# Optimization experiments

Hardware: AMD Instinct MI355X
Metric: run time of the kernel (lower is better)

## Reference

```python
import jax, jax.numpy as jnp
import numpy as np

B, N, H, NH, P = 32, 400, 512, 8, 3
DK = H // NH
SCALE = DK ** -0.5
EPS = 1e-5


def _ln(x, g, b):
    m = jnp.mean(x, axis=-1, keepdims=True)
    v = jnp.mean((x - m) ** 2, axis=-1, keepdims=True)
    return (x - m) * jax.lax.rsqrt(v + EPS) * g + b


def _split(x):  # [B,N,H] -> [B,h,N,dk]
    return x.reshape(x.shape[0], x.shape[1], NH, DK).transpose(0, 2, 1, 3)


def _merge(x):  # [B,h,N,dk] -> [B,N,H]
    return x.transpose(0, 2, 1, 3).reshape(x.shape[0], x.shape[2], H)


def _attn(q, k, v, mask):
    s = jnp.einsum('bhid,bhjd->bhij', q, k) * SCALE
    s = s * (1.0 + mask[:, None])  # learned multiplicative prior mask
    p = jax.nn.softmax(s, axis=-1)
    return jnp.einsum('bhij,bhjd->bhid', p, v)


def _weight_gen(pri, z, C, wq, keys, wf, bf):
    # pooled token query attends over the num_priors prior matrices
    qv = jnp.mean(z @ wq, axis=1)  # [B,H]
    aw = jax.nn.softmax((qv @ keys.T) * (H ** -0.5), axis=-1)  # [B,P]
    w = jnp.einsum('bp,bpij->bij', aw, pri)  # [B,N,N] fused prior mask
    fused = jnp.einsum('bij,bjh->bih', C, z) @ wf + bf  # [B,N,H] neighborhood fusion
    return w, aw, fused


def _ffn(x, w1, b1, w2, b2):
    return jax.nn.gelu(x @ w1 + b1, approximate=False) @ w2 + b2


def _forward(x_FC, x_SC, pri_FC, pri_SC, FC, SC, dw,
             ln_attn_FC_g, ln_attn_FC_b, ln_attn_SC_g, ln_attn_SC_b,
             ln_ffn_FC_g, ln_ffn_FC_b, ln_ffn_SC_g, ln_ffn_SC_b,
             qkv_FC_w, qkv_SC_w,
             ffn_FC_w1, ffn_FC_b1, ffn_FC_w2, ffn_FC_b2,
             ffn_SC_w1, ffn_SC_b1, ffn_SC_w2, ffn_SC_b2,
             wg_q_w, wg_keys, wg_fuse_w, wg_fuse_b,
             dist_in_FC_w, dist_in_FC_b, dist_in_SC_w, dist_in_SC_b,
             dist_out_FC_w, dist_out_FC_b, dist_out_SC_w, dist_out_SC_b):
    z_FC = _ln(x_FC, ln_attn_FC_g, ln_attn_FC_b)
    z_SC = _ln(x_SC, ln_attn_SC_g, ln_attn_SC_b)
    q_FC, k_FC, v_FC = [_split(t) for t in jnp.split(z_FC @ qkv_FC_w, 3, axis=-1)]
    q_SC, k_SC, v_SC = [_split(t) for t in jnp.split(z_SC @ qkv_SC_w, 3, axis=-1)]
    w_FC, aw_FC, fused_FC = _weight_gen(pri_FC, z_FC, FC, wg_q_w, wg_keys, wg_fuse_w, wg_fuse_b)
    w_SC, aw_SC, fused_SC = _weight_gen(pri_SC, z_SC, SC, wg_q_w, wg_keys, wg_fuse_w, wg_fuse_b)
    ctx_FC = _merge(_attn(q_FC, k_FC, v_FC, w_FC))
    ctx_SC = _merge(_attn(q_SC, k_SC, v_SC, w_SC))
    attn_out_FC = x_FC + ctx_FC + fused_FC
    attn_out_SC = x_SC + ctx_SC + fused_SC
    x_FC_new = attn_out_FC + _ffn(_ln(attn_out_FC, ln_ffn_FC_g, ln_ffn_FC_b), ffn_FC_w1, ffn_FC_b1, ffn_FC_w2, ffn_FC_b2)
    x_SC_new = attn_out_SC + _ffn(_ln(attn_out_SC, ln_ffn_SC_g, ln_ffn_SC_b), ffn_SC_w1, ffn_SC_b1, ffn_SC_w2, ffn_SC_b2)
    wf, ws = dw[0], dw[1]
    proj_FC = x_FC_new @ dist_in_FC_w + dist_in_FC_b
    proj_SC = x_SC_new @ dist_in_SC_w + dist_in_SC_b
    l_FC = jax.nn.log_softmax(proj_FC.reshape(-1, H), axis=-1)
    l_SC = jax.nn.log_softmax(proj_SC.reshape(-1, H), axis=-1)
    p_FC = jnp.exp(l_FC)
    p_SC = jnp.exp(l_SC)
    rows = jnp.float32(l_FC.shape[0])
    kl_FC = jnp.sum(p_SC * (l_SC - l_FC)) / rows  # KLDiv(batchmean)(l_FC, p_SC)
    kl_SC = jnp.sum(p_FC * (l_FC - l_SC)) / rows
    x_FC_out = (1.0 - wf) * x_FC_new + wf * (proj_FC @ dist_out_FC_w + dist_out_FC_b)
    x_SC_out = (1.0 - ws) * x_SC_new + ws * (proj_SC @ dist_out_SC_w + dist_out_SC_b)
    distill_loss = 0.5 * (kl_FC * wf + kl_SC * ws)
    return (x_FC_out, x_SC_out, distill_loss, aw_FC, aw_SC)


def setup_inputs() -> dict:
    key = jax.random.key(0)
    ks = jax.random.split(key, 24)
    init = lambda k, shape: 0.02 * jax.random.normal(k, shape, jnp.float32)
    d = {}
    d['x_FC'] = jax.random.normal(ks[0], (B, N, H), jnp.float32)
    d['x_SC'] = jax.random.normal(ks[1], (B, N, H), jnp.float32)
    d['pri_FC'] = jax.random.uniform(ks[2], (B, P, N, N), jnp.float32)
    d['pri_SC'] = jax.random.uniform(ks[3], (B, P, N, N), jnp.float32)
    d['FC'] = jax.random.uniform(ks[4], (B, N, N), jnp.float32)
    d['SC'] = jax.random.uniform(ks[5], (B, N, N), jnp.float32)
    d['dw'] = jnp.array([0.5, 0.5], jnp.float32)
    for nm in ['ln_attn_FC', 'ln_attn_SC', 'ln_ffn_FC', 'ln_ffn_SC']:
        d[nm + '_g'] = jnp.ones((H,), jnp.float32)
        d[nm + '_b'] = jnp.zeros((H,), jnp.float32)
    d['qkv_FC_w'] = init(ks[6], (H, 3 * H))
    d['qkv_SC_w'] = init(ks[7], (H, 3 * H))
    d['ffn_FC_w1'] = init(ks[8], (H, 4 * H)); d['ffn_FC_b1'] = jnp.zeros((4 * H,), jnp.float32)
    d['ffn_FC_w2'] = init(ks[9], (4 * H, H)); d['ffn_FC_b2'] = jnp.zeros((H,), jnp.float32)
    d['ffn_SC_w1'] = init(ks[10], (H, 4 * H)); d['ffn_SC_b1'] = jnp.zeros((4 * H,), jnp.float32)
    d['ffn_SC_w2'] = init(ks[11], (4 * H, H)); d['ffn_SC_b2'] = jnp.zeros((H,), jnp.float32)
    d['wg_q_w'] = init(ks[12], (H, H))
    d['wg_keys'] = init(ks[13], (P, H))
    d['wg_fuse_w'] = init(ks[14], (H, H)); d['wg_fuse_b'] = jnp.zeros((H,), jnp.float32)
    d['dist_in_FC_w'] = init(ks[15], (H, H)); d['dist_in_FC_b'] = jnp.zeros((H,), jnp.float32)
    d['dist_in_SC_w'] = init(ks[16], (H, H)); d['dist_in_SC_b'] = jnp.zeros((H,), jnp.float32)
    d['dist_out_FC_w'] = init(ks[17], (H, H)); d['dist_out_FC_b'] = jnp.zeros((H,), jnp.float32)
    d['dist_out_SC_w'] = init(ks[18], (H, H)); d['dist_out_SC_b'] = jnp.zeros((H,), jnp.float32)
    return d


def reference(x_FC, x_SC, pri_FC, pri_SC, FC, SC, dw,
              ln_attn_FC_g, ln_attn_FC_b, ln_attn_SC_g, ln_attn_SC_b,
              ln_ffn_FC_g, ln_ffn_FC_b, ln_ffn_SC_g, ln_ffn_SC_b,
              qkv_FC_w, qkv_SC_w,
              ffn_FC_w1, ffn_FC_b1, ffn_FC_w2, ffn_FC_b2,
              ffn_SC_w1, ffn_SC_b1, ffn_SC_w2, ffn_SC_b2,
              wg_q_w, wg_keys, wg_fuse_w, wg_fuse_b,
              dist_in_FC_w, dist_in_FC_b, dist_in_SC_w, dist_in_SC_b,
              dist_out_FC_w, dist_out_FC_b, dist_out_SC_w, dist_out_SC_b):
    return _forward(x_FC, x_SC, pri_FC, pri_SC, FC, SC, dw,
                    ln_attn_FC_g, ln_attn_FC_b, ln_attn_SC_g, ln_attn_SC_b,
                    ln_ffn_FC_g, ln_ffn_FC_b, ln_ffn_SC_g, ln_ffn_SC_b,
                    qkv_FC_w, qkv_SC_w,
                    ffn_FC_w1, ffn_FC_b1, ffn_FC_w2, ffn_FC_b2,
                    ffn_SC_w1, ffn_SC_b1, ffn_SC_w2, ffn_SC_b2,
                    wg_q_w, wg_keys, wg_fuse_w, wg_fuse_b,
                    dist_in_FC_w, dist_in_FC_b, dist_in_SC_w, dist_in_SC_b,
                    dist_out_FC_w, dist_out_FC_b, dist_out_SC_w, dist_out_SC_b)
```

## Files before the change

### kernel.cpp

```cpp
#include <hip/hip_runtime.h>
#include <hip/hip_bf16.h>
#include <math.h>

typedef __hip_bfloat16 bf16;

#define B_  32
#define N_  400
#define H_  512
#define NH_ 8
#define DK_ 64
#define P_  3
#define BN_ (B_*N_)
#define H3_ 1536
#define H4_ 2048

#define GLD16(g, l) __builtin_amdgcn_global_load_lds( \
    (__attribute__((address_space(1))) void*)(g), \
    (__attribute__((address_space(3))) void*)(l), 16, 0, 0)

__device__ __forceinline__ float b2f(bf16 v){ return __bfloat162float(v); }
__device__ __forceinline__ bf16  f2b(float v){ return __float2bfloat16(v); }
__device__ __forceinline__ float bfu(unsigned short u){ return __uint_as_float(((unsigned int)u)<<16); }
__device__ __forceinline__ unsigned short f2bu(float v){
  union { bf16 b; unsigned short u; } cv; cv.b = __float2bfloat16(v); return cv.u;
}
__device__ __forceinline__ bool is_f32(const void* gref){
  return *(const unsigned int*)gref == 0x3F800000u;
}
__device__ __forceinline__ float ldRaw(const void* p, long i, bool f32){
  return f32 ? ((const float*)p)[i] : b2f(((const bf16*)p)[i]);
}
__device__ __forceinline__ void stRaw(void* p, long i, float v, bool f32){
  if (f32) ((float*)p)[i] = v; else ((bf16*)p)[i] = f2b(v);
}

__device__ __forceinline__ float waveSum(float v){
  #pragma unroll
  for (int o=32;o>0;o>>=1) v += __shfl_xor(v,o,64);
  return v;
}
__device__ __forceinline__ float waveMax(float v){
  #pragma unroll
  for (int o=32;o>0;o>>=1) v = fmaxf(v,__shfl_xor(v,o,64));
  return v;
}
__device__ __forceinline__ float blockSum(float v, float* wred){
  v = waveSum(v);
  int w = threadIdx.x>>6, l = threadIdx.x&63;
  if (l==0) wred[w]=v;
  __syncthreads();
  float r = wred[0]+wred[1]+wred[2]+wred[3];
  __syncthreads();
  return r;
}
__device__ __forceinline__ float blockMax(float v, float* wred){
  v = waveMax(v);
  int w = threadIdx.x>>6, l = threadIdx.x&63;
  if (l==0) wred[w]=v;
  __syncthreads();
  float r = fmaxf(fmaxf(wred[0],wred[1]),fmaxf(wred[2],wred[3]));
  __syncthreads();
  return r;
}

template<int XMODE>
__global__ __launch_bounds__(256)
void ln_kernel(const void* __restrict__ x, const void* __restrict__ g,
               const void* __restrict__ bb, bf16* __restrict__ out,
               const void* __restrict__ gref)
{
  __shared__ float wred[4];
  const bool F32 = is_f32(gref);
  long row = blockIdx.x;
  int t = threadIdx.x;
  long base = row*H_;
  float v0, v1;
  if (XMODE==0){ v0 = ldRaw(x, base+t, F32); v1 = ldRaw(x, base+t+256, F32); }
  else         { v0 = b2f(((const bf16*)x)[base+t]); v1 = b2f(((const bf16*)x)[base+t+256]); }
  float mean = blockSum(v0+v1, wred) * (1.f/512.f);
  float d0 = v0-mean, d1 = v1-mean;
  float var = blockSum(d0*d0+d1*d1, wred) * (1.f/512.f);
  float rs = rsqrtf(var + 1e-5f);
  bf16* orow = out + base;
  orow[t]     = f2b(d0*rs*ldRaw(g,t,F32)     + ldRaw(bb,t,F32));
  orow[t+256] = f2b(d1*rs*ldRaw(g,t+256,F32) + ldRaw(bb,t+256,F32));
}

struct TC6 {
  const float* W[6];
  bf16* WT[6];
  int K[6]; int N[6]; int base[6];
};
__global__ __launch_bounds__(256)
void tc6_kernel(TC6 p)
{
  __shared__ float tile[32][33];
  int gt = blockIdx.x;
  int seg = 0;
  #pragma unroll
  for (int i=1;i<6;++i) if (gt >= p.base[i]) seg = i;
  int lt = gt - p.base[seg];
  int K = p.K[seg], N = p.N[seg];
  int ntx = N >> 5;
  int n0 = (lt % ntx)*32, k0 = (lt / ntx)*32;
  const float* W = p.W[seg];
  bf16* WT = p.WT[seg];
  int t = threadIdx.x;
  int c = t & 31, r = t >> 5;
  #pragma unroll
  for (int q=0;q<4;++q){
    int k = r + q*8;
    tile[k][c] = W[(long)(k0+k)*N + n0 + c];
  }
  __syncthreads();
  #pragma unroll
  for (int q=0;q<4;++q){
    int nn = r + q*8;
    WT[(long)(n0+nn)*K + k0 + c] = f2b(tile[c][nn]);
  }
}

__global__ __launch_bounds__(256)
void ztrans_kernel(const bf16* __restrict__ ZB, bf16* __restrict__ ZBT)
{
  __shared__ unsigned short tile[32][33];
  int j0 = blockIdx.x*32, h0 = blockIdx.y*32, b = blockIdx.z;
  int t = threadIdx.x;
  int c = t & 31, r = t >> 5;
  const unsigned short* src = (const unsigned short*)(ZB + (long)b*N_*H_);
  #pragma unroll
  for (int p=0;p<4;++p){
    int j = j0 + r + p*8;
    unsigned short v = 0;
    if (j < 400) v = src[(long)j*H_ + h0 + c];
    tile[r+p*8][c] = v;
  }
  __syncthreads();
  unsigned short* dst = (unsigned short*)(ZBT + (long)b*512*416);
  #pragma unroll
  for (int p=0;p<4;++p){
    int hh = r + p*8;
    dst[(long)(h0+hh)*416 + j0 + c] = tile[c][hh];
  }
}

__global__ __launch_bounds__(256)
void cconv_kernel(const float* __restrict__ C, bf16* __restrict__ CB)
{
  long u = ((long)blockIdx.x*256 + threadIdx.x)*8;
  int b = (int)(u / (512*416));
  int rem = (int)(u - (long)b*(512*416));
  int r = rem / 416, c = rem % 416;
  ushort4 lo = {0,0,0,0}, hi = {0,0,0,0};
  if (r < 400 && c < 400){
    const float* p = C + (long)b*160000 + r*400 + c;
    float4 f0 = *(const float4*)p;
    float4 f1 = *(const float4*)(p+4);
    lo.x=f2bu(f0.x); lo.y=f2bu(f0.y); lo.z=f2bu(f0.z); lo.w=f2bu(f0.w);
    hi.x=f2bu(f1.x); hi.y=f2bu(f1.y); hi.z=f2bu(f1.z); hi.w=f2bu(f1.w);
  }
  *(ushort4*)((unsigned short*)CB + u)     = lo;
  *(ushort4*)((unsigned short*)CB + u + 4) = hi;
}

__global__ __launch_bounds__(256)
void vtrans_kernel(const bf16* __restrict__ qkv, bf16* __restrict__ vtg)
{
  __shared__ unsigned short tile[32][33];
  int j0 = blockIdx.x*32, d0 = blockIdx.y*32, bh = blockIdx.z;
  int b = bh >> 3, h = bh & 7;
  int t = threadIdx.x;
  int c = t & 31, r = t >> 5;
  const unsigned short* src = (const unsigned short*)(qkv + (long)b*N_*H3_ + 1024 + h*64 + d0);
  #pragma unroll
  for (int p=0;p<4;++p){
    int j = j0 + r + p*8;
    unsigned short v = 0;
    if (j < 400) v = src[(long)j*H3_ + c];
    tile[r+p*8][c] = v;
  }
  __syncthreads();
  unsigned short* dst = (unsigned short*)(vtg + (long)bh*64*416);
  #pragma unroll
  for (int p=0;p<4;++p){
    int dd = r + p*8;
    dst[(long)(d0+dd)*416 + j0 + c] = tile[c][dd];
  }
}

template<int MI,int ACT,int RES,int OMODE>
__global__ __launch_bounds__(256)
void mgemm_kernel(const bf16* __restrict__ A, const bf16* __restrict__ BT,
                  const float* __restrict__ bias, const bf16* __restrict__ res,
                  void* __restrict__ out, long oOff,
                  int M, int K, int Nn,
                  long sA, long sW, long sO,
                  const float* __restrict__ dwp, int dwidx)
{
  typedef __attribute__((ext_vector_type(8))) short bf16x8;
  typedef __attribute__((ext_vector_type(4))) float f32x4;
  constexpr int BM = MI*32;
  __shared__ unsigned short As[2][BM*32];
  __shared__ unsigned short Bs[2][128*32];
  int t = threadIdx.x;
  int w = t >> 6, l = t & 63;
  int wm = (w >> 1)*(MI*16), wn = (w & 1)*64;
  int m0 = blockIdx.y*BM, n0 = blockIdx.x*128;
  long zA = (long)blockIdx.z*sA;
  const bf16* Ab = A + zA;
  const bf16* Bb = BT + (long)blockIdx.z*sW;
  long zO = (long)blockIdx.z*sO;
  f32x4 acc[MI][4] = {};
  int lrow = l & 15, lkc = l >> 4;
  int srow = t >> 2, skc = t & 3;
  int sk = (skc ^ ((srow >> 1) & 3))*8;
  int ck = (lkc ^ ((lrow >> 1) & 3))*8;
  int nk = K >> 5;
  int buf = 0;

  #pragma unroll
  for (int half=0; half<MI/2; ++half){
    const unsigned short* gA = (const unsigned short*)Ab + (long)(m0+srow+half*64)*K + sk;
    GLD16(gA, &As[0][w*512 + half*2048]);
  }
  #pragma unroll
  for (int half=0; half<2; ++half){
    const unsigned short* gB = (const unsigned short*)Bb + (long)(n0+srow+half*64)*K + sk;
    GLD16(gB, &Bs[0][w*512 + half*2048]);
  }
  __syncthreads();
  for (int kt=0; kt<nk; ++kt){
    if (kt+1 < nk){
      int k1 = (kt+1) << 5;
      #pragma unroll
      for (int half=0; half<MI/2; ++half){
        const unsigned short* gA = (const unsigned short*)Ab + (long)(m0+srow+half*64)*K + k1 + sk;
        GLD16(gA, &As[buf^1][w*512 + half*2048]);
      }
      #pragma unroll
      for (int half=0; half<2; ++half){
        const unsigned short* gB = (const unsigned short*)Bb + (long)(n0+srow+half*64)*K + k1 + sk;
        GLD16(gB, &Bs[buf^1][w*512 + half*2048]);
      }
    }
    bf16x8 af[MI], bf_[4];
    #pragma unroll
    for (int i=0;i<MI;++i) af[i]  = *(const bf16x8*)&As[buf][(wm + i*16 + lrow)*32 + ck];
    #pragma unroll
    for (int i=0;i<4;++i)  bf_[i] = *(const bf16x8*)&Bs[buf][(wn + i*16 + lrow)*32 + ck];
    #pragma unroll
    for (int mi=0;mi<MI;++mi)
      #pragma unroll
      for (int ni=0;ni<4;++ni)
        acc[mi][ni] = __builtin_amdgcn_mfma_f32_16x16x32_bf16(bf_[ni], af[mi], acc[mi][ni], 0, 0, 0);
    __syncthreads();
    buf ^= 1;
  }
  float wbl = (RES==2) ? dwp[dwidx] : 0.f;
  #pragma unroll
  for (int mi=0;mi<MI;++mi){
    int gm = m0 + wm + mi*16 + lrow;
    if (gm >= M) continue;
    #pragma unroll
    for (int ni=0;ni<4;++ni){
      int gnb = n0 + wn + ni*16 + lkc*4;
      long o = zO + (long)gm*Nn + gnb;
      float v0 = acc[mi][ni][0], v1 = acc[mi][ni][1], v2 = acc[mi][ni][2], v3 = acc[mi][ni][3];
      if (bias){
        float4 bv = *(const float4*)&bias[gnb];
        v0 += bv.x; v1 += bv.y; v2 += bv.z; v3 += bv.w;
      }
      if (ACT==1){
        v0 = 0.5f*v0*(1.f + erff(v0*0.70710678118654752f));
        v1 = 0.5f*v1*(1.f + erff(v1*0.70710678118654752f));
        v2 = 0.5f*v2*(1.f + erff(v2*0.70710678118654752f));
        v3 = 0.5f*v3*(1.f + erff(v3*0.70710678118654752f));
      }
      if (RES==1){
        ushort4 r4 = *(const ushort4*)((const unsigned short*)res + o);
        v0 += bfu(r4.x); v1 += bfu(r4.y); v2 += bfu(r4.z); v3 += bfu(r4.w);
      }
      if (RES==2){
        ushort4 r4 = *(const ushort4*)((const unsigned short*)res + o);
        v0 = (1.f-wbl)*bfu(r4.x) + wbl*v0;
        v1 = (1.f-wbl)*bfu(r4.y) + wbl*v1;
        v2 = (1.f-wbl)*bfu(r4.z) + wbl*v2;
        v3 = (1.f-wbl)*bfu(r4.w) + wbl*v3;
      }
      if (OMODE==0){
        ushort4 o4;
        o4.x = f2bu(v0); o4.y = f2bu(v1); o4.z = f2bu(v2); o4.w = f2bu(v3);
        *(ushort4*)((unsigned short*)out + o) = o4;
      } else {
        *(float4*)((float*)out + oOff + o) = make_float4(v0,v1,v2,v3);
      }
    }
  }
}

__global__ __launch_bounds__(256)
void zbar_kernel(const bf16* __restrict__ Z, float* __restrict__ zbar)
{
  __shared__ float red[256];
  int hc = blockIdx.x, b = blockIdx.y;
  int t = threadIdx.x;
  int col = hc*64 + (t & 63), ns = t >> 6;
  const bf16* p = Z + (long)b*N_*H_ + (long)ns*100*H_ + col;
  float s = 0.f;
  for (int n=0;n<100;++n) s += b2f(p[(long)n*H_]);
  red[t] = s;
  __syncthreads();
  if (t < 64){
    float tot = red[t]+red[t+64]+red[t+128]+red[t+192];
    zbar[b*512 + hc*64 + t] = tot * (1.f/400.f);
  }
}

__global__ __launch_bounds__(256)
void qv_kernel(const float* __restrict__ zbar, const void* __restrict__ wq,
               float* __restrict__ qv, const void* __restrict__ gref)
{
  __shared__ float red[256];
  const bool F32 = is_f32(gref);
  int ch = blockIdx.x, b = blockIdx.y;
  int t = threadIdx.x;
  int col = ch*32 + (t & 31), ks = t >> 5;
  const float* zb = zbar + b*512;
  float s = 0.f;
  int k0 = ks*64;
  for (int k=0;k<64;++k)
    s = fmaf(zb[k0+k], ldRaw(wq, (long)(k0+k)*512 + col, F32), s);
  red[t] = s;
  __syncthreads();
  if (t < 32){
    float q = 0.f;
    #pragma unroll
    for (int i=0;i<8;++i) q += red[t + i*32];
    qv[b*512 + ch*32 + t] = q;
  }
}

__global__ __launch_bounds__(256)
void aw_kernel(const float* __restrict__ qv, const void* __restrict__ keys,
               float* __restrict__ awf, void* __restrict__ outbase, long offAw,
               const void* __restrict__ gref)
{
  __shared__ float wred[4];
  const bool F32 = is_f32(gref);
  int b = blockIdx.x, t = threadIdx.x;
  const float* q = qv + b*512;
  float lg[3];
  #pragma unroll
  for (int p=0;p<3;++p){
    float part = q[t]*ldRaw(keys, p*512+t, F32) + q[t+256]*ldRaw(keys, p*512+t+256, F32);
    lg[p] = blockSum(part, wred) * 0.04419417382415922f;
  }
  float m = fmaxf(lg[0], fmaxf(lg[1], lg[2]));
  float e0 = expf(lg[0]-m), e1 = expf(lg[1]-m), e2 = expf(lg[2]-m);
  float inv = 1.f/(e0+e1+e2);
  if (t<3){
    float a = (t==0?e0:(t==1?e1:e2))*inv;
    awf[b*3+t] = a;
    stRaw(outbase, offAw + b*3 + t, a, F32);
  }
}

__global__ __launch_bounds__(256)
void wcomb_kernel(const void* __restrict__ pri, const float* __restrict__ awf,
                  bf16* __restrict__ WM, const void* __restrict__ gref)
{
  const bool F32 = is_f32(gref);
  long u = (long)blockIdx.x*256 + threadIdx.x;
  long e0 = u*4;
  int b = (int)(e0 / 160000);
  long r = e0 - (long)b*160000;
  float a0 = awf[b*3+0], a1 = awf[b*3+1], a2 = awf[b*3+2];
  float o0,o1,o2,o3;
  if (F32){
    const float* p0 = (const float*)pri + (long)b*3*160000 + r;
    float4 a = *(const float4*)(p0);
    float4 c = *(const float4*)(p0 + 160000);
    float4 d = *(const float4*)(p0 + 320000);
    o0 = a0*a.x + a1*c.x + a2*d.x;
    o1 = a0*a.y + a1*c.y + a2*d.y;
    o2 = a0*a.z + a1*c.z + a2*d.z;
    o3 = a0*a.w + a1*c.w + a2*d.w;
  } else {
    const bf16* p0 = (const bf16*)pri + (long)b*3*160000 + r;
    ushort4 a = *(const ushort4*)(p0);
    ushort4 c = *(const ushort4*)(p0 + 160000);
    ushort4 d = *(const ushort4*)(p0 + 320000);
    o0 = a0*bfu(a.x) + a1*bfu(c.x) + a2*bfu(d.x);
    o1 = a0*bfu(a.y) + a1*bfu(c.y) + a2*bfu(d.y);
    o2 = a0*bfu(a.z) + a1*bfu(c.z) + a2*bfu(d.z);
    o3 = a0*bfu(a.w) + a1*bfu(c.w) + a2*bfu(d.w);
  }
  ushort4 o;
  o.x = f2bu(o0); o.y = f2bu(o1); o.z = f2bu(o2); o.w = f2bu(o3);
  *(ushort4*)(WM + e0) = o;
}

__global__ __launch_bounds__(128)
void attn_kernel(const bf16* __restrict__ qkv, const bf16* __restrict__ wm,
                 const bf16* __restrict__ vtg, const void* __restrict__ x,
                 const bf16* __restrict__ fused, bf16* __restrict__ aout,
                 const void* __restrict__ gref)
{
  typedef __attribute__((ext_vector_type(8))) short bf16x8;
  typedef __attribute__((ext_vector_type(4))) float f32x4;
  __shared__ unsigned short Pbuf[2][2][16*40];
  const bool F32 = is_f32(gref);
  int t = threadIdx.x, wv = t >> 6, l = t & 63;
  int h = blockIdx.x, b = blockIdx.y;
  int qt = blockIdx.z*2 + wv;
  if (qt >= 25) return;
  int lr = l & 15, lg = l >> 4;
  int i0 = qt*16;
  const bf16* qb = qkv + (long)b*N_*H3_ + h*64;
  const bf16* kb = qb + 512;
  const bf16* wrow = wm + (long)b*N_*N_;
  const bf16* vt = vtg + (long)(b*NH_ + h)*64*416;
  bf16x8 qf0 = *(const bf16x8*)(qb + (long)(i0+lr)*H3_ + lg*8);
  bf16x8 qf1 = *(const bf16x8*)(qb + (long)(i0+lr)*H3_ + 32 + lg*8);
  float rm = -1e30f, rl = 0.f;
  f32x4 o[4] = {};
  #pragma unroll
  for (int w=0; w<13; ++w){
    int t0 = 2*w, t1 = 2*w+1;
    f32x4 s0, s1;
    {
      bf16x8 kf0 = *(const bf16x8*)(kb + (long)(t0*16+lr)*H3_ + lg*8);
      bf16x8 kf1 = *(const bf16x8*)(kb + (long)(t0*16+lr)*H3_ + 32 + lg*8);
      f32x4 st = {0.f,0.f,0.f,0.f};
      st = __builtin_amdgcn_mfma_f32_16x16x32_bf16(kf0, qf0, st, 0,0,0);
      st = __builtin_amdgcn_mfma_f32_16x16x32_bf16(kf1, qf1, st, 0,0,0);
      uint2 w4 = *(const uint2*)(wrow + (long)(i0+lr)*400 + t0*16 + lg*4);
      s0[0] = st[0]*0.125f*(1.f + bfu((unsigned short)(w4.x & 0xffffu)));
      s0[1] = st[1]*0.125f*(1.f + bfu((unsigned short)(w4.x >> 16)));
      s0[2] = st[2]*0.125f*(1.f + bfu((unsigned short)(w4.y & 0xffffu)));
      s0[3] = st[3]*0.125f*(1.f + bfu((unsigned short)(w4.y >> 16)));
    }
    if (t1 < 25){
      bf16x8 kf0 = *(const bf16x8*)(kb + (long)(t1*16+lr)*H3_ + lg*8);
      bf16x8 kf1 = *(const bf16x8*)(kb + (long)(t1*16+lr)*H3_ + 32 + lg*8);
      f32x4 st = {0.f,0.f,0.f,0.f};
      st = __builtin_amdgcn_mfma_f32_16x16x32_bf16(kf0, qf0, st, 0,0,0);
      st = __builtin_amdgcn_mfma_f32_16x16x32_bf16(kf1, qf1, st, 0,0,0);
      uint2 w4 = *(const uint2*)(wrow + (long)(i0+lr)*400 + t1*16 + lg*4);
      s1[0] = st[0]*0.125f*(1.f + bfu((unsigned short)(w4.x & 0xffffu)));
      s1[1] = st[1]*0.125f*(1.f + bfu((unsigned short)(w4.x >> 16)));
      s1[2] = st[2]*0.125f*(1.f + bfu((unsigned short)(w4.y & 0xffffu)));
      s1[3] = st[3]*0.125f*(1.f + bfu((unsigned short)(w4.y >> 16)));
    } else {
      s1[0]=s1[1]=s1[2]=s1[3] = -1e30f;
    }
    float tm = fmaxf(fmaxf(fmaxf(s0[0],s0[1]), fmaxf(s0[2],s0[3])),
                     fmaxf(fmaxf(s1[0],s1[1]), fmaxf(s1[2],s1[3])));
    tm = fmaxf(tm, __shfl_xor(tm, 16));
    tm = fmaxf(tm, __shfl_xor(tm, 32));
    float mn = fmaxf(rm, tm);
    float sc = __expf(rm - mn);
    unsigned pk0x, pk0y, pk1x = 0u, pk1y = 0u;
    float ls = 0.f;
    {
      unsigned u0 = f2bu(__expf(s0[0]-mn)), u1 = f2bu(__expf(s0[1]-mn));
      unsigned u2 = f2bu(__expf(s0[2]-mn)), u3 = f2bu(__expf(s0[3]-mn));
      pk0x = u0 | (u1<<16); pk0y = u2 | (u3<<16);
      ls += __uint_as_float(u0<<16) + __uint_as_float(u1<<16)
          + __uint_as_float(u2<<16) + __uint_as_float(u3<<16);
    }
    if (t1 < 25){
      unsigned u0 = f2bu(__expf(s1[0]-mn)), u1 = f2bu(__expf(s1[1]-mn));
      unsigned u2 = f2bu(__expf(s1[2]-mn)), u3 = f2bu(__expf(s1[3]-mn));
      pk1x = u0 | (u1<<16); pk1y = u2 | (u3<<16);
      ls += __uint_as_float(u0<<16) + __uint_as_float(u1<<16)
          + __uint_as_float(u2<<16) + __uint_as_float(u3<<16);
    }
    ls += __shfl_xor(ls, 16);
    ls += __shfl_xor(ls, 32);
    rl = rl*sc + ls;
    rm = mn;
    unsigned short* pb = Pbuf[wv][w & 1];
    *(uint2*)&pb[lr*40 + lg*4]      = make_uint2(pk0x, pk0y);
    *(uint2*)&pb[lr*40 + 16 + lg*4] = make_uint2(pk1x, pk1y);
    bf16x8 pa = *(const bf16x8*)&pb[lr*40 + lg*8];
    float sq0 = __shfl(sc, lg*4 + 0);
    float sq1 = __shfl(sc, lg*4 + 1);
    float sq2 = __shfl(sc, lg*4 + 2);
    float sq3 = __shfl(sc, lg*4 + 3);
    #pragma unroll
    for (int dt=0; dt<4; ++dt){
      o[dt][0] *= sq0; o[dt][1] *= sq1; o[dt][2] *= sq2; o[dt][3] *= sq3;
      bf16x8 vf = *(const bf16x8*)(vt + (long)(dt*16+lr)*416 + w*32 + lg*8);
      o[dt] = __builtin_amdgcn_mfma_f32_16x16x32_bf16(pa, vf, o[dt], 0,0,0);
    }
  }
  float invl = 1.f/rl;
  #pragma unroll
  for (int q=0;q<4;++q){
    float iv = __shfl(invl, lg*4 + q);
    long gi = (long)(b*N_ + i0 + lg*4 + q);
    #pragma unroll
    for (int dt=0;dt<4;++dt){
      long oi = gi*H_ + h*64 + dt*16 + lr;
      float xv = F32 ? ((const float*)x)[oi] : b2f(((const bf16*)x)[oi]);
      float fv = b2f(fused[oi]);
      aout[oi] = f2b(o[dt][q]*iv + xv + fv);
    }
  }
}

__global__ __launch_bounds__(256)
void kl_rows_kernel(const bf16* __restrict__ pF, const bf16* __restrict__ pS,
                    float2* __restrict__ rowpart)
{
  __shared__ float wred[4];
  long row = blockIdx.x;
  int t = threadIdx.x;
  const bf16* fr = pF + row*512;
  const bf16* sr = pS + row*512;
  float f0 = b2f(fr[t]), f1 = b2f(fr[t+256]), s0 = b2f(sr[t]), s1 = b2f(sr[t+256]);
  float mF = blockMax(fmaxf(f0,f1), wred);
  float mS = blockMax(fmaxf(s0,s1), wred);
  float sumF = blockSum(__expf(f0-mF)+__expf(f1-mF), wred);
  float sumS = blockSum(__expf(s0-mS)+__expf(s1-mS), wred);
  float lseF = mF + __logf(sumF), lseS = mS + __logf(sumS);
  float lF0 = f0-lseF, lF1 = f1-lseF, lS0 = s0-lseS, lS1 = s1-lseS;
  float pS0 = __expf(lS0), pS1 = __expf(lS1), pF0 = __expf(lF0), pF1 = __expf(lF1);
  float a  = pS0*(lS0-lF0) + pS1*(lS1-lF1);
  float bb = pF0*(lF0-lS0) + pF1*(lF1-lS1);
  a  = blockSum(a,  wred);
  bb = blockSum(bb, wred);
  if (t==0) rowpart[row] = make_float2(a, bb);
}

__global__ __launch_bounds__(256)
void kl_final_kernel(const float2* __restrict__ rowpart, const void* __restrict__ dw,
                     void* __restrict__ outbase, long offLoss,
                     const void* __restrict__ gref)
{
  __shared__ float wred[4];
  const bool F32 = is_f32(gref);
  int t = threadIdx.x;
  float sa=0.f, sb=0.f;
  for (int i=t;i<BN_;i+=256){ float2 v = rowpart[i]; sa+=v.x; sb+=v.y; }
  sa = blockSum(sa, wred);
  sb = blockSum(sb, wred);
  if (t==0){
    float wf = ldRaw(dw,0,F32), ws = ldRaw(dw,1,F32);
    float loss = 0.5f*((sa/12800.f)*wf + (sb/12800.f)*ws);
    stRaw(outbase, offLoss, loss, F32);
  }
}

#define OFF_ZB    0L
#define OFF_QKV   13107200L
#define OFF_FUSED 52428800L
#define OFF_WM    65536000L
#define OFF_CZ    75776000L
#define OFF_PROJ0 88883200L
#define OFF_PROJ1 101990400L
#define OFF_QKVT  115097600L
#define OFF_W1T   116670464L
#define OFF_W2T   118767616L
#define OFF_FUT   120864768L
#define OFF_DIT   121389056L
#define OFF_DOT   121913344L
#define OFF_ZBT   122437632L
#define OFF_ZBAR  136069120L
#define OFF_AWF   136134656L
#define OFF_ROWP  136135680L
#define OFF_VTG   136238080L
#define OFF_QV    149869568L

extern "C" void kernel_launch(void* const* d_in, const int* in_sizes, int n_in,
                              void* d_out, int out_size, void* d_ws, size_t ws_size,
                              hipStream_t stream)
{
  (void)in_sizes; (void)n_in; (void)out_size; (void)ws_size;
  const void* x[2]    = {d_in[0],  d_in[1]};
  const void* pri[2]  = {d_in[2],  d_in[3]};
  const float* Cm[2]  = {(const float*)d_in[4], (const float*)d_in[5]};
  const float* dwf    =  (const float*)d_in[6];
  const void* lnag[2] = {d_in[7],  d_in[9]};
  const void* lnab[2] = {d_in[8],  d_in[10]};
  const void* lnfg[2] = {d_in[11], d_in[13]};
  const void* lnfb[2] = {d_in[12], d_in[14]};
  const float* qkvw[2]= {(const float*)d_in[15], (const float*)d_in[16]};
  const float* fw1[2] = {(const float*)d_in[17], (const float*)d_in[21]};
  const float* fb1[2] = {(const float*)d_in[18], (const float*)d_in[22]};
  const float* fw2[2] = {(const float*)d_in[19], (const float*)d_in[23]};
  const float* fb2[2] = {(const float*)d_in[20], (const float*)d_in[24]};
  const void* wgq     =  d_in[25];
  const void* wgk     =  d_in[26];
  const float* wgfw   =  (const float*)d_in[27];
  const float* wgfb   =  (const float*)d_in[28];
  const float* diw[2] = {(const float*)d_in[29], (const float*)d_in[31]};
  const float* dib[2] = {(const float*)d_in[30], (const float*)d_in[32]};
  const float* dow[2] = {(const float*)d_in[33], (const float*)d_in[35]};
  const float* dob[2] = {(const float*)d_in[34], (const float*)d_in[36]};
  const void* gref    =  d_in[7];

  char* ws = (char*)d_ws;
  bf16*  ZB    = (bf16*)(ws + OFF_ZB);
  bf16*  LN2   = (bf16*)(ws + OFF_ZB);
  bf16*  XNEW  = (bf16*)(ws + OFF_ZB);
  bf16*  QKV   = (bf16*)(ws + OFF_QKV);
  bf16*  HH    = (bf16*)(ws + OFF_QKV);
  bf16*  FUSED = (bf16*)(ws + OFF_FUSED);
  bf16*  WM    = (bf16*)(ws + OFF_WM);
  bf16*  CZ    = (bf16*)(ws + OFF_CZ);
  bf16*  AOUT  = (bf16*)(ws + OFF_CZ);
  bf16*  PROJ[2] = {(bf16*)(ws + OFF_PROJ0), (bf16*)(ws + OFF_PROJ1)};
  bf16*  QKVT  = (bf16*)(ws + OFF_QKVT);
  bf16*  W1T   = (bf16*)(ws + OFF_W1T);
  bf16*  W2T   = (bf16*)(ws + OFF_W2T);
  bf16*  FUT   = (bf16*)(ws + OFF_FUT);
  bf16*  DIT   = (bf16*)(ws + OFF_DIT);
  bf16*  DOT   = (bf16*)(ws + OFF_DOT);
  bf16*  ZBT   = (bf16*)(ws + OFF_ZBT);
  bf16*  VTG   = (bf16*)(ws + OFF_VTG);
  bf16*  CB    = (bf16*)(ws + OFF_VTG);
  float* ZBAR  = (float*)(ws + OFF_ZBAR);
  float* AWF   = (float*)(ws + OFF_AWF);
  float2* ROWP = (float2*)(ws + OFF_ROWP);
  float* QV    = (float*)(ws + OFF_QV);

  const long offX[2]  = {0L, 6553600L};
  const long offLoss  = 13107200L;
  const long offAw[2] = {13107201L, 13107297L};

  for (int s=0; s<2; ++s){
    TC6 tp;
    tp.W[0]=qkvw[s]; tp.WT[0]=QKVT; tp.K[0]=512;  tp.N[0]=1536;
    tp.W[1]=fw1[s];  tp.WT[1]=W1T;  tp.K[1]=512;  tp.N[1]=2048;
    tp.W[2]=fw2[s];  tp.WT[2]=W2T;  tp.K[2]=2048; tp.N[2]=512;
    tp.W[3]=wgfw;    tp.WT[3]=FUT;  tp.K[3]=512;  tp.N[3]=512;
    tp.W[4]=diw[s];  tp.WT[4]=DIT;  tp.K[4]=512;  tp.N[4]=512;
    tp.W[5]=dow[s];  tp.WT[5]=DOT;  tp.K[5]=512;  tp.N[5]=512;
    tp.base[0]=0; tp.base[1]=768; tp.base[2]=1792; tp.base[3]=2816;
    tp.base[4]=3072; tp.base[5]=3328;
    tc6_kernel<<<3584,256,0,stream>>>(tp);
    ln_kernel<0><<<BN_,256,0,stream>>>(x[s], lnag[s], lnab[s], ZB, gref);
    zbar_kernel<<<dim3(8,B_),256,0,stream>>>(ZB, ZBAR);
    ztrans_kernel<<<dim3(13,16,32),256,0,stream>>>(ZB, ZBT);
    cconv_kernel<<<3328,256,0,stream>>>(Cm[s], CB);
    mgemm_kernel<4,0,0,0><<<dim3(12,100,1),256,0,stream>>>(
        ZB, QKVT, nullptr, nullptr, QKV, 0, BN_, 512, H3_, 0,0,0, nullptr,0);
    qv_kernel<<<dim3(16,B_),256,0,stream>>>(ZBAR, wgq, QV, gref);
    aw_kernel<<<B_,256,0,stream>>>(QV, wgk, AWF, d_out, offAw[s], gref);
    wcomb_kernel<<<5000,256,0,stream>>>(pri[s], AWF, WM, gref);
    mgemm_kernel<4,0,0,0><<<dim3(4,4,32),256,0,stream>>>(
        CB, ZBT, nullptr, nullptr, CZ, 0, 400, 416, 512,
        212992L, 212992L, 204800L, nullptr,0);
    mgemm_kernel<2,0,0,0><<<dim3(4,200,1),256,0,stream>>>(
        CZ, FUT, wgfb, nullptr, FUSED, 0, BN_, 512, 512, 0,0,0, nullptr,0);
    vtrans_kernel<<<dim3(13,2,256),256,0,stream>>>(QKV, VTG);
    attn_kernel<<<dim3(NH_,B_,13),128,0,stream>>>(QKV, WM, VTG, x[s], FUSED, AOUT, gref);
    ln_kernel<1><<<BN_,256,0,stream>>>(AOUT, lnfg[s], lnfb[s], LN2, gref);
    mgemm_kernel<4,1,0,0><<<dim3(16,100,1),256,0,stream>>>(
        LN2, W1T, fb1[s], nullptr, HH, 0, BN_, 512, H4_, 0,0,0, nullptr,0);
    mgemm_kernel<2,0,1,0><<<dim3(4,200,1),256,0,stream>>>(
        HH, W2T, fb2[s], AOUT, XNEW, 0, BN_, 2048, 512, 0,0,0, nullptr,0);
    mgemm_kernel<2,0,0,0><<<dim3(4,200,1),256,0,stream>>>(
        XNEW, DIT, dib[s], nullptr, PROJ[s], 0, BN_, 512, 512, 0,0,0, nullptr,0);
    mgemm_kernel<2,0,2,1><<<dim3(4,200,1),256,0,stream>>>(
        PROJ[s], DOT, dob[s], XNEW, d_out, offX[s], BN_, 512, 512, 0,0,0, dwf, s);
  }
  kl_rows_kernel<<<BN_,256,0,stream>>>(PROJ[0], PROJ[1], ROWP);
  kl_final_kernel<<<1,256,0,stream>>>(ROWP, dwf, d_out, offLoss, gref);
}
```

Baseline: 918.8 us.

## Triple-buffer GEMM LDS tiles with explicit vmcnt waits and MFMA priority

Moves the generic MFMA GEMM from double to triple buffering in LDS, issuing global-to-LDS loads two K-tiles ahead. Per-tile __syncthreads is replaced by precise s_waitcnt vmcnt counts plus raw barriers, so one tile's loads can remain in flight while another is computed. It also raises wave priority around the MFMA block. The cost is 50% more LDS per block, which may lower occupancy, and correctness now depends on the hand-counted vmcnt values.

New measurement: 920.5 us. About the same (+0.2%).

```diff
diff --git a/kernel.cpp b/kernel.cpp
--- a/kernel.cpp
+++ b/kernel.cpp
@@ -200,8 +200,9 @@
   typedef __attribute__((ext_vector_type(8))) short bf16x8;
   typedef __attribute__((ext_vector_type(4))) float f32x4;
   constexpr int BM = MI*32;
-  __shared__ unsigned short As[2][BM*32];
-  __shared__ unsigned short Bs[2][128*32];
+  constexpr int LPT = MI/2 + 2;
+  __shared__ unsigned short As[3][BM*32];
+  __shared__ unsigned short Bs[3][128*32];
   int t = threadIdx.x;
   int w = t >> 6, l = t & 63;
   int wm = (w >> 1)*(MI*16), wn = (w & 1)*64;
@@ -216,45 +217,45 @@
   int sk = (skc ^ ((srow >> 1) & 3))*8;
   int ck = (lkc ^ ((lrow >> 1) & 3))*8;
   int nk = K >> 5;
-  int buf = 0;
-
-  #pragma unroll
-  for (int half=0; half<MI/2; ++half){
-    const unsigned short* gA = (const unsigned short*)Ab + (long)(m0+srow+half*64)*K + sk;
-    GLD16(gA, &As[0][w*512 + half*2048]);
-  }
-  #pragma unroll
-  for (int half=0; half<2; ++half){
-    const unsigned short* gB = (const unsigned short*)Bb + (long)(n0+srow+half*64)*K + sk;
-    GLD16(gB, &Bs[0][w*512 + half*2048]);
-  }
-  __syncthreads();
+
+  auto STAGE = [&](int tile, int bufi){
+    int kk = tile << 5;
+    #pragma unroll
+    for (int half=0; half<MI/2; ++half){
+      const unsigned short* gA = (const unsigned short*)Ab + (long)(m0+srow+half*64)*K + kk + sk;
+      GLD16(gA, &As[bufi][w*512 + half*2048]);
+    }
+    #pragma unroll
+    for (int half=0; half<2; ++half){
+      const unsigned short* gB = (const unsigned short*)Bb + (long)(n0+srow+half*64)*K + kk + sk;
+      GLD16(gB, &Bs[bufi][w*512 + half*2048]);
+    }
+  };
+
+  STAGE(0, 0);
+  if (nk > 1) STAGE(1, 1);
   for (int kt=0; kt<nk; ++kt){
-    if (kt+1 < nk){
-      int k1 = (kt+1) << 5;
-      #pragma unroll
-      for (int half=0; half<MI/2; ++half){
-        const unsigned short* gA = (const unsigned short*)Ab + (long)(m0+srow+half*64)*K + k1 + sk;
-        GLD16(gA, &As[buf^1][w*512 + half*2048]);
-      }
-      #pragma unroll
-      for (int half=0; half<2; ++half){
-        const unsigned short* gB = (const unsigned short*)Bb + (long)(n0+srow+half*64)*K + k1 + sk;
-        GLD16(gB, &Bs[buf^1][w*512 + half*2048]);
-      }
-    }
+    int cur = kt % 3;
+    if (kt+2 < nk) STAGE(kt+2, (kt+2)%3);
+    if (kt+2 < nk)      asm volatile("s_waitcnt vmcnt(%0)" :: "i"(2*LPT) : "memory");
+    else if (kt+1 < nk) asm volatile("s_waitcnt vmcnt(%0)" :: "i"(LPT)   : "memory");
+    else                asm volatile("s_waitcnt vmcnt(0)" ::: "memory");
+    __builtin_amdgcn_s_barrier();
+    asm volatile("" ::: "memory");
     bf16x8 af[MI], bf_[4];
     #pragma unroll
-    for (int i=0;i<MI;++i) af[i]  = *(const bf16x8*)&As[buf][(wm + i*16 + lrow)*32 + ck];
-    #pragma unroll
-    for (int i=0;i<4;++i)  bf_[i] = *(const bf16x8*)&Bs[buf][(wn + i*16 + lrow)*32 + ck];
+    for (int i=0;i<MI;++i) af[i]  = *(const bf16x8*)&As[cur][(wm + i*16 + lrow)*32 + ck];
+    #pragma unroll
+    for (int i=0;i<4;++i)  bf_[i] = *(const bf16x8*)&Bs[cur][(wn + i*16 + lrow)*32 + ck];
+    __builtin_amdgcn_s_setprio(1);
     #pragma unroll
     for (int mi=0;mi<MI;++mi)
       #pragma unroll
       for (int ni=0;ni<4;++ni)
         acc[mi][ni] = __builtin_amdgcn_mfma_f32_16x16x32_bf16(bf_[ni], af[mi], acc[mi][ni], 0, 0, 0);
-    __syncthreads();
-    buf ^= 1;
+    __builtin_amdgcn_s_setprio(0);
+    asm volatile("" ::: "memory");
+    __builtin_amdgcn_s_barrier();
   }
   float wbl = (RES==2) ? dwp[dwidx] : 0.f;
   #pragma unroll
```
